# Performance work log

Hardware: AMD Instinct MI355X
Metric: run time of the kernel (lower is better)

The kernel has to match this reference:

```python
import jax, jax.numpy as jnp
import numpy as np

LN_EPS = 1e-5


def setup_inputs() -> dict:
    key = jax.random.key(0)
    ks = jax.random.split(key, 8)
    N, E, DIN, DOUT = 50000, 800000, 128, 128
    s = 1.0 / np.sqrt(DIN)
    return {
        "vertex_features": jax.random.normal(ks[0], (N, DIN), jnp.float32),
        "edge_index": jax.random.randint(ks[1], (2, E), 0, N, jnp.int32),
        "W_edge": jax.random.normal(ks[2], (DIN, DOUT), jnp.float32) * s,
        "b_edge": jnp.zeros((DOUT,), jnp.float32),
        "W1": jax.random.normal(ks[3], (DIN + DOUT, DOUT), jnp.float32) * (1.0 / np.sqrt(DIN + DOUT)),
        "b1": jnp.zeros((DOUT,), jnp.float32),
        "ln_gamma": jnp.ones((DOUT,), jnp.float32),
        "ln_beta": jnp.zeros((DOUT,), jnp.float32),
        "W2": jax.random.normal(ks[4], (DOUT, DOUT), jnp.float32) * (1.0 / np.sqrt(DOUT)),
        "b2": jnp.zeros((DOUT,), jnp.float32),
    }


def layer_norm(x, gamma, beta):
    mu = jnp.mean(x, axis=-1, keepdims=True)
    var = jnp.mean(jnp.square(x - mu), axis=-1, keepdims=True)
    return (x - mu) * jax.lax.rsqrt(var + LN_EPS) * gamma + beta


def reference(vertex_features, edge_index, W_edge, b_edge, W1, b1, ln_gamma, ln_beta, W2, b2):
    N = vertex_features.shape[0]
    src, dst = edge_index[0], edge_index[1]
    # gather-subtract: [E, DIN]
    edge_feats = vertex_features[src] - vertex_features[dst]
    # edge linear: [E, DOUT]
    edge_feats = edge_feats @ W_edge + b_edge
    # scatter_max by dst -> [N, DOUT]; empty segments get -inf -> replace with 0
    agg = jax.ops.segment_max(edge_feats, dst, num_segments=N)
    agg = jnp.where(jnp.isfinite(agg), agg, 0.0)
    combined = jnp.concatenate([vertex_features, agg], axis=-1)  # [N, DIN+DOUT]
    h = combined @ W1 + b1
    h = jax.nn.relu(layer_norm(h, ln_gamma, ln_beta))
    return h @ W2 + b2
```

## Files before the change

### kernel.cpp

```cpp
#include <hip/hip_runtime.h>
#include <stdint.h>

#define DIN 128
#define DOUT 128
#define LN_EPS 1e-5f
#define CAP 64

typedef __attribute__((ext_vector_type(8))) short bf16x8;
typedef __attribute__((ext_vector_type(4))) float f32x4;

__device__ __forceinline__ unsigned short f2bf(float f) {
  uint32_t u = __float_as_uint(f);
  uint32_t r = (u + 0x7fffu + ((u >> 16) & 1u)) >> 16;
  return (unsigned short)r;
}
__device__ __forceinline__ float bf2f(uint32_t lo16) {
  return __uint_as_float(lo16 << 16);
}
__device__ __forceinline__ uint32_t pack2(unsigned short a, unsigned short b) {
  return (uint32_t)a | ((uint32_t)b << 16);
}
__device__ __forceinline__ uint32_t cvtpk_bf16(float lo, float hi) {
  uint32_t r;
  asm volatile("v_cvt_pk_bf16_f32 %0, %1, %2" : "=v"(r) : "v"(lo), "v"(hi));
  return r;
}

__global__ __launch_bounds__(256) void k_prep(
    const float* __restrict__ We, const float* __restrict__ W1,
    const float* __restrict__ W2, char* __restrict__ img,
    int4* __restrict__ degv4, int nv4, int wblk) {
  if (blockIdx.x >= wblk) {
    int i = (blockIdx.x - wblk) * 256 + threadIdx.x;
    if (i < nv4) degv4[i] = make_int4(0, 0, 0, 0);
    return;
  }
  int tid = blockIdx.x * 256 + threadIdx.x;
  const int total = 128 * 128 + 256 * 128 + 128 * 128;
  for (int i = tid; i < total; i += wblk * 256) {
    int off;
    float v;
    if (i < 16384) {
      int k = i >> 7, c = i & 127;
      v = We[k * 128 + c];
      off = c * 256 + ((k * 2) ^ ((c & 7) << 4));
    } else if (i < 49152) {
      int j = i - 16384;
      int k = j >> 7, c = j & 127;
      v = W1[k * 128 + c];
      off = 32768 + c * 512 + ((k * 2) ^ ((c & 7) << 4));
    } else {
      int j = i - 49152;
      int k = j >> 7, c = j & 127;
      v = W2[k * 128 + c];
      off = 98304 + c * 256 + ((k * 2) ^ ((c & 7) << 4));
    }
    *(unsigned short*)(img + off) = f2bf(v);
  }
}

__global__ __launch_bounds__(256, 1) void k_gemm_histplace(
    const float* __restrict__ vf, const char* __restrict__ wimg,
    short* __restrict__ P16, short* __restrict__ vf16, int N,
    const int* __restrict__ ei, int* __restrict__ deg,
    unsigned short* __restrict__ ssrc, int E, int nblk) {
  __shared__ char Wet[32768];
  if (blockIdx.x >= nblk) {
    int e = (blockIdx.x - nblk) * 256 + threadIdx.x;
    if (e < E) {
      int s = ei[e];
      int d = ei[E + e];
      int r = atomicAdd(&deg[d], 1);
      if (r < CAP) ssrc[(size_t)d * CAP + r] = (unsigned short)s;
    }
    return;
  }
  {
    const uint4* src = (const uint4*)wimg;
    for (int i = threadIdx.x; i < 2048; i += 256) *(uint4*)(Wet + i * 16) = src[i];
  }
  int wave = threadIdx.x >> 6, lane = threadIdx.x & 63;
  int l15 = lane & 15, lq = lane >> 4;
  int row0 = blockIdx.x * 256 + wave * 64;
  int rs[4];
#pragma unroll
  for (int m = 0; m < 4; ++m) rs[m] = min(row0 + m * 16 + l15, N - 1);

  f32x4 acc[4][8];
#pragma unroll
  for (int m = 0; m < 4; ++m)
#pragma unroll
    for (int n = 0; n < 8; ++n) acc[m][n] = (f32x4)0.f;

  float4 pf0[4], pf1[4];
#pragma unroll
  for (int m = 0; m < 4; ++m) {
    const float* p = vf + (size_t)rs[m] * DIN + lq * 8;
    pf0[m] = *(const float4*)p;
    pf1[m] = *(const float4*)(p + 4);
  }
  __syncthreads();

#pragma unroll
  for (int ks = 0; ks < 4; ++ks) {
    bf16x8 afr[4];
#pragma unroll
    for (int m = 0; m < 4; ++m) {
      uint4 st;
      st.x = cvtpk_bf16(pf0[m].x, pf0[m].y);
      st.y = cvtpk_bf16(pf0[m].z, pf0[m].w);
      st.z = cvtpk_bf16(pf1[m].x, pf1[m].y);
      st.w = cvtpk_bf16(pf1[m].z, pf1[m].w);
      afr[m] = *(bf16x8*)&st;
      int row = row0 + m * 16 + l15;
      if (row < N)
        *(uint4*)(vf16 + (size_t)row * DIN + ks * 32 + lq * 8) = st;
    }
    if (ks < 3) {
#pragma unroll
      for (int m = 0; m < 4; ++m) {
        const float* p = vf + (size_t)rs[m] * DIN + (ks + 1) * 32 + lq * 8;
        pf0[m] = *(const float4*)p;
        pf1[m] = *(const float4*)(p + 4);
      }
    }
    int kb = ks * 64 + lq * 16;
#pragma unroll
    for (int n = 0; n < 8; ++n) {
      int c = n * 16 + l15;
      bf16x8 b = *(const bf16x8*)(Wet + c * 256 + (kb ^ ((c & 7) << 4)));
#pragma unroll
      for (int m = 0; m < 4; ++m)
        acc[m][n] = __builtin_amdgcn_mfma_f32_16x16x32_bf16(afr[m], b, acc[m][n], 0, 0, 0);
    }
  }
#pragma unroll
  for (int m = 0; m < 4; ++m) {
    int rbase = row0 + m * 16 + lq * 4;
#pragma unroll
    for (int n = 0; n < 8; ++n) {
      int col = n * 16 + l15;
#pragma unroll
      for (int reg = 0; reg < 4; ++reg) {
        int row = rbase + reg;
        if (row < N) P16[(size_t)row * DOUT + col] = (short)f2bf(acc[m][n][reg]);
      }
    }
  }
}

__global__ __launch_bounds__(256) void k_segmax(const short* __restrict__ P16,
                                                const int* __restrict__ degA,
                                                const unsigned short* __restrict__ ssrc,
                                                const float* __restrict__ b_edge,
                                                short* __restrict__ A16, int N) {
  int lane = threadIdx.x & 63;
  int l16 = lane & 15;
  int v = blockIdx.x * 16 + (threadIdx.x >> 4);
  if (v >= N) return;
  int deg = min(degA[v], CAP);
  size_t beg = (size_t)v * CAP;
  float m[8];
#pragma unroll
  for (int j = 0; j < 8; ++j) m[j] = -__builtin_inff();
  for (int r = 0; r < deg; r += 16) {
    int cnt = min(16, deg - r);
    int sv = (l16 < cnt) ? (int)ssrc[beg + r + l16] : 0;
#pragma unroll 2
    for (int i = 0; i < cnt; ++i) {
      int s = __shfl(sv, (lane & 48) + i, 64);
      uint4 p = *(const uint4*)(P16 + (size_t)s * DOUT + l16 * 8);
      m[0] = fmaxf(m[0], bf2f(p.x & 0xffffu));
      m[1] = fmaxf(m[1], bf2f(p.x >> 16));
      m[2] = fmaxf(m[2], bf2f(p.y & 0xffffu));
      m[3] = fmaxf(m[3], bf2f(p.y >> 16));
      m[4] = fmaxf(m[4], bf2f(p.z & 0xffffu));
      m[5] = fmaxf(m[5], bf2f(p.z >> 16));
      m[6] = fmaxf(m[6], bf2f(p.w & 0xffffu));
      m[7] = fmaxf(m[7], bf2f(p.w >> 16));
    }
  }
  uint4 pv = *(const uint4*)(P16 + (size_t)v * DOUT + l16 * 8);
  float4 be0 = *(const float4*)(b_edge + l16 * 8);
  float4 be1 = *(const float4*)(b_edge + l16 * 8 + 4);
  float pvf[8] = {bf2f(pv.x & 0xffffu), bf2f(pv.x >> 16), bf2f(pv.y & 0xffffu),
                  bf2f(pv.y >> 16),     bf2f(pv.z & 0xffffu), bf2f(pv.z >> 16),
                  bf2f(pv.w & 0xffffu), bf2f(pv.w >> 16)};
  float bev[8] = {be0.x, be0.y, be0.z, be0.w, be1.x, be1.y, be1.z, be1.w};
  uint32_t o[4];
#pragma unroll
  for (int j = 0; j < 4; ++j) {
    float a0 = (deg > 0) ? (m[2 * j] - pvf[2 * j] + bev[2 * j]) : 0.f;
    float a1 = (deg > 0) ? (m[2 * j + 1] - pvf[2 * j + 1] + bev[2 * j + 1]) : 0.f;
    o[j] = pack2(f2bf(a0), f2bf(a1));
  }
  *(uint4*)(A16 + (size_t)v * DOUT + l16 * 8) = *(uint4*)o;
}

__global__ __launch_bounds__(256, 1) void k_mlp12(
    const short* __restrict__ vf16, const short* __restrict__ A16,
    const char* __restrict__ wimg, const float* __restrict__ b1,
    const float* __restrict__ gamma, const float* __restrict__ beta,
    const float* __restrict__ b2, float* __restrict__ out, int N) {
  __shared__ char lds[98304];
  char* W1t = lds;
  char* W2t = lds + 65536;
  {
    const uint4* src = (const uint4*)(wimg + 32768);
    for (int i = threadIdx.x; i < 6144; i += 256) *(uint4*)(lds + i * 16) = src[i];
  }
  int wave = threadIdx.x >> 6, lane = threadIdx.x & 63;
  int l15 = lane & 15, lq = lane >> 4;
  int row0 = blockIdx.x * 256 + wave * 64;
  int rs[4];
#pragma unroll
  for (int m = 0; m < 4; ++m) rs[m] = min(row0 + m * 16 + l15, N - 1);
  float b1v[8], gv[8], bev[8], b2v[8];
#pragma unroll
  for (int n = 0; n < 8; ++n) {
    int c = n * 16 + l15;
    b1v[n] = b1[c];
    gv[n] = gamma[c];
    bev[n] = beta[c];
    b2v[n] = b2[c];
  }
  f32x4 acc[4][8];
#pragma unroll
  for (int m = 0; m < 4; ++m)
#pragma unroll
    for (int n = 0; n < 8; ++n) acc[m][n] = (f32x4)0.f;

  uint4 pa[4];
#pragma unroll
  for (int m = 0; m < 4; ++m)
    pa[m] = *(const uint4*)(vf16 + (size_t)rs[m] * DIN + lq * 8);
  __syncthreads();

#pragma unroll
  for (int ks = 0; ks < 8; ++ks) {
    bf16x8 afr[4];
#pragma unroll
    for (int m = 0; m < 4; ++m) afr[m] = *(bf16x8*)&pa[m];
    if (ks < 7) {
      int ks1 = ks + 1;
      const short* srcb = (ks1 < 4) ? vf16 : A16;
      int chunk = (ks1 < 4) ? ks1 : ks1 - 4;
#pragma unroll
      for (int m = 0; m < 4; ++m)
        pa[m] = *(const uint4*)(srcb + (size_t)rs[m] * DIN + chunk * 32 + lq * 8);
    }
    int kb = ks * 64 + lq * 16;
#pragma unroll
    for (int n = 0; n < 8; ++n) {
      int c = n * 16 + l15;
      bf16x8 b = *(const bf16x8*)(W1t + c * 512 + (kb ^ ((c & 7) << 4)));
#pragma unroll
      for (int m = 0; m < 4; ++m)
        acc[m][n] = __builtin_amdgcn_mfma_f32_16x16x32_bf16(afr[m], b, acc[m][n], 0, 0, 0);
    }
  }
  __syncthreads();

#pragma unroll
  for (int m = 0; m < 4; ++m) {
#pragma unroll
    for (int n = 0; n < 8; ++n)
#pragma unroll
      for (int reg = 0; reg < 4; ++reg) acc[m][n][reg] += b1v[n];
    float s[4], sq[4];
#pragma unroll
    for (int reg = 0; reg < 4; ++reg) {
      s[reg] = 0.f;
      sq[reg] = 0.f;
#pragma unroll
      for (int n = 0; n < 8; ++n) {
        float h = acc[m][n][reg];
        s[reg] += h;
        sq[reg] += h * h;
      }
    }
#pragma unroll
    for (int mm = 1; mm < 16; mm <<= 1) {
#pragma unroll
      for (int reg = 0; reg < 4; ++reg) {
        s[reg] += __shfl_xor(s[reg], mm, 64);
        sq[reg] += __shfl_xor(sq[reg], mm, 64);
      }
    }
#pragma unroll
    for (int reg = 0; reg < 4; ++reg) {
      float mu = s[reg] * (1.f / 128.f);
      float var = sq[reg] * (1.f / 128.f) - mu * mu;
      float rsn = rsqrtf(var + LN_EPS);
      int rr = wave * 64 + m * 16 + lq * 4 + reg;
#pragma unroll
      for (int n = 0; n < 8; ++n) {
        float o = fmaxf(fmaf((acc[m][n][reg] - mu) * rsn, gv[n], bev[n]), 0.f);
        int c = n * 16 + l15;
        *(unsigned short*)(W1t + rr * 256 + ((c * 2) ^ ((rr & 7) << 4))) = f2bf(o);
      }
    }
  }
  __syncthreads();

  f32x4 acc2[4][8];
#pragma unroll
  for (int m = 0; m < 4; ++m)
#pragma unroll
    for (int n = 0; n < 8; ++n) acc2[m][n] = (f32x4)0.f;
#pragma unroll
  for (int ks = 0; ks < 4; ++ks) {
    int kb = ks * 64 + lq * 16;
    bf16x8 a2[4];
#pragma unroll
    for (int m = 0; m < 4; ++m) {
      int rr = wave * 64 + m * 16 + l15;
      a2[m] = *(const bf16x8*)(W1t + rr * 256 + (kb ^ ((rr & 7) << 4)));
    }
#pragma unroll
    for (int n = 0; n < 8; ++n) {
      int c = n * 16 + l15;
      bf16x8 b = *(const bf16x8*)(W2t + c * 256 + (kb ^ ((c & 7) << 4)));
#pragma unroll
      for (int m = 0; m < 4; ++m)
        acc2[m][n] = __builtin_amdgcn_mfma_f32_16x16x32_bf16(a2[m], b, acc2[m][n], 0, 0, 0);
    }
  }
#pragma unroll
  for (int m = 0; m < 4; ++m) {
    int rbase = row0 + m * 16 + lq * 4;
#pragma unroll
    for (int n = 0; n < 8; ++n) {
      int col = n * 16 + l15;
#pragma unroll
      for (int reg = 0; reg < 4; ++reg) {
        int row = rbase + reg;
        if (row < N) out[(size_t)row * DOUT + col] = acc2[m][n][reg] + b2v[n];
      }
    }
  }
}

extern "C" void kernel_launch(void* const* d_in, const int* in_sizes, int n_in,
                              void* d_out, int out_size, void* d_ws, size_t ws_size,
                              hipStream_t stream) {
  const float* vf     = (const float*)d_in[0];
  const int*   ei     = (const int*)d_in[1];
  const float* W_edge = (const float*)d_in[2];
  const float* b_edge = (const float*)d_in[3];
  const float* W1     = (const float*)d_in[4];
  const float* b1     = (const float*)d_in[5];
  const float* gamma  = (const float*)d_in[6];
  const float* beta   = (const float*)d_in[7];
  const float* W2     = (const float*)d_in[8];
  const float* b2     = (const float*)d_in[9];
  float* out = (float*)d_out;

  int N = in_sizes[0] / DIN;
  int E = in_sizes[1] / 2;
  int nblk = (N + 255) / 256;
  int eblk = (E + 255) / 256;

  char* ws = (char*)d_ws;
  size_t seg16 = (size_t)N * DOUT * sizeof(short);
  short* P16  = (short*)ws;
  short* vf16 = (short*)(ws + seg16);
  short* A16  = (short*)(ws + 2 * seg16);
  char*  wimg = ws + 3 * seg16;
  int*   deg  = (int*)(ws + 3 * seg16 + 131072);
  unsigned short* ssrc = (unsigned short*)(deg + ((N + 3) & ~3));

  int nv4 = (N + 3) / 4;
  int zblk = (nv4 + 255) / 256;
  k_prep<<<64 + zblk, 256, 0, stream>>>(W_edge, W1, W2, wimg, (int4*)deg, nv4, 64);
  k_gemm_histplace<<<nblk + eblk, 256, 0, stream>>>(vf, wimg, P16, vf16, N, ei,
                                                    deg, ssrc, E, nblk);
  k_segmax<<<(N + 15) / 16, 256, 0, stream>>>(P16, deg, ssrc, b_edge, A16, N);
  k_mlp12<<<nblk, 256, 0, stream>>>(vf16, A16, wimg, b1, gamma, beta, b2, out, N);
}
```

Before: 114.5 us.

## Privatize edge histogram and bucket lists per XCD to avoid cross-die atomics

The shared degree counters and per-destination source lists are replaced with one copy per XCD, selected by reading the hardware XCC id register. Atomics are relaxed at workgroup scope, which is meant to remove cross-die coherence traffic and contention on the global counters. The segment-max kernel then walks all eight buckets per vertex and sums their counts. Edge blocks are also launched ahead of GEMM blocks. In exchange, workspace and zeroing grow eightfold, the source-list scatter spreads over a much larger footprint, and the reduction loop has more overhead per vertex.

```diff
diff --git a/kernel.cpp b/kernel.cpp
--- a/kernel.cpp
+++ b/kernel.cpp
@@ -4,7 +4,10 @@
 #define DIN 128
 #define DOUT 128
 #define LN_EPS 1e-5f
-#define CAP 64
+#define CAPX 64
+#define NXCD 8
+
+#define XCC_ID_ENC (20 | (0 << 6) | ((4 - 1) << 11))
 
 typedef __attribute__((ext_vector_type(8))) short bf16x8;
 typedef __attribute__((ext_vector_type(4))) float f32x4;
@@ -62,26 +65,30 @@
 __global__ __launch_bounds__(256, 1) void k_gemm_histplace(
     const float* __restrict__ vf, const char* __restrict__ wimg,
     short* __restrict__ P16, short* __restrict__ vf16, int N,
-    const int* __restrict__ ei, int* __restrict__ deg,
-    unsigned short* __restrict__ ssrc, int E, int nblk) {
+    const int* __restrict__ ei, int* __restrict__ deg8,
+    unsigned short* __restrict__ ssrc8, int E, int eblk) {
   __shared__ char Wet[32768];
-  if (blockIdx.x >= nblk) {
-    int e = (blockIdx.x - nblk) * 256 + threadIdx.x;
+  if (blockIdx.x < eblk) {
+    int e = blockIdx.x * 256 + threadIdx.x;
     if (e < E) {
       int s = ei[e];
       int d = ei[E + e];
-      int r = atomicAdd(&deg[d], 1);
-      if (r < CAP) ssrc[(size_t)d * CAP + r] = (unsigned short)s;
+      uint32_t xcc = ((uint32_t)__builtin_amdgcn_s_getreg(XCC_ID_ENC)) & (NXCD - 1);
+      int r = __hip_atomic_fetch_add(&deg8[(size_t)xcc * N + d], 1,
+                                     __ATOMIC_RELAXED, __HIP_MEMORY_SCOPE_WORKGROUP);
+      if (r < CAPX)
+        ssrc8[((size_t)xcc * N + d) * CAPX + r] = (unsigned short)s;
     }
     return;
   }
+  int bid = blockIdx.x - eblk;
   {
     const uint4* src = (const uint4*)wimg;
     for (int i = threadIdx.x; i < 2048; i += 256) *(uint4*)(Wet + i * 16) = src[i];
   }
   int wave = threadIdx.x >> 6, lane = threadIdx.x & 63;
   int l15 = lane & 15, lq = lane >> 4;
-  int row0 = blockIdx.x * 256 + wave * 64;
+  int row0 = bid * 256 + wave * 64;
   int rs[4];
 #pragma unroll
   for (int m = 0; m < 4; ++m) rs[m] = min(row0 + m * 16 + l15, N - 1);
@@ -150,34 +157,39 @@
 }
 
 __global__ __launch_bounds__(256) void k_segmax(const short* __restrict__ P16,
-                                                const int* __restrict__ degA,
-                                                const unsigned short* __restrict__ ssrc,
+                                                const int* __restrict__ deg8,
+                                                const unsigned short* __restrict__ ssrc8,
                                                 const float* __restrict__ b_edge,
                                                 short* __restrict__ A16, int N) {
   int lane = threadIdx.x & 63;
   int l16 = lane & 15;
   int v = blockIdx.x * 16 + (threadIdx.x >> 4);
   if (v >= N) return;
-  int deg = min(degA[v], CAP);
-  size_t beg = (size_t)v * CAP;
+  int cx = (l16 < NXCD) ? deg8[(size_t)l16 * N + v] : 0;
   float m[8];
 #pragma unroll
   for (int j = 0; j < 8; ++j) m[j] = -__builtin_inff();
-  for (int r = 0; r < deg; r += 16) {
-    int cnt = min(16, deg - r);
-    int sv = (l16 < cnt) ? (int)ssrc[beg + r + l16] : 0;
+  int total = 0;
+  for (int x = 0; x < NXCD; ++x) {
+    int cnt = min(__shfl(cx, (lane & 48) + x, 64), CAPX);
+    total += cnt;
+    size_t base = ((size_t)x * N + v) * CAPX;
+    for (int r = 0; r < cnt; r += 16) {
+      int c2 = min(16, cnt - r);
+      int sv = (l16 < c2) ? (int)ssrc8[base + r + l16] : 0;
 #pragma unroll 2
-    for (int i = 0; i < cnt; ++i) {
-      int s = __shfl(sv, (lane & 48) + i, 64);
-      uint4 p = *(const uint4*)(P16 + (size_t)s * DOUT + l16 * 8);
-      m[0] = fmaxf(m[0], bf2f(p.x & 0xffffu));
-      m[1] = fmaxf(m[1], bf2f(p.x >> 16));
-      m[2] = fmaxf(m[2], bf2f(p.y & 0xffffu));
-      m[3] = fmaxf(m[3], bf2f(p.y >> 16));
-      m[4] = fmaxf(m[4], bf2f(p.z & 0xffffu));
-      m[5] = fmaxf(m[5], bf2f(p.z >> 16));
-      m[6] = fmaxf(m[6], bf2f(p.w & 0xffffu));
-      m[7] = fmaxf(m[7], bf2f(p.w >> 16));
+      for (int i = 0; i < c2; ++i) {
+        int s = __shfl(sv, (lane & 48) + i, 64);
+        uint4 p = *(const uint4*)(P16 + (size_t)s * DOUT + l16 * 8);
+        m[0] = fmaxf(m[0], bf2f(p.x & 0xffffu));
+        m[1] = fmaxf(m[1], bf2f(p.x >> 16));
+        m[2] = fmaxf(m[2], bf2f(p.y & 0xffffu));
+        m[3] = fmaxf(m[3], bf2f(p.y >> 16));
+        m[4] = fmaxf(m[4], bf2f(p.z & 0xffffu));
+        m[5] = fmaxf(m[5], bf2f(p.z >> 16));
+        m[6] = fmaxf(m[6], bf2f(p.w & 0xffffu));
+        m[7] = fmaxf(m[7], bf2f(p.w >> 16));
+      }
     }
   }
   uint4 pv = *(const uint4*)(P16 + (size_t)v * DOUT + l16 * 8);
@@ -190,8 +202,8 @@
   uint32_t o[4];
 #pragma unroll
   for (int j = 0; j < 4; ++j) {
-    float a0 = (deg > 0) ? (m[2 * j] - pvf[2 * j] + bev[2 * j]) : 0.f;
-    float a1 = (deg > 0) ? (m[2 * j + 1] - pvf[2 * j + 1] + bev[2 * j + 1]) : 0.f;
+    float a0 = (total > 0) ? (m[2 * j] - pvf[2 * j] + bev[2 * j]) : 0.f;
+    float a1 = (total > 0) ? (m[2 * j + 1] - pvf[2 * j + 1] + bev[2 * j + 1]) : 0.f;
     o[j] = pack2(f2bf(a0), f2bf(a1));
   }
   *(uint4*)(A16 + (size_t)v * DOUT + l16 * 8) = *(uint4*)o;
@@ -367,14 +379,15 @@
   short* vf16 = (short*)(ws + seg16);
   short* A16  = (short*)(ws + 2 * seg16);
   char*  wimg = ws + 3 * seg16;
-  int*   deg  = (int*)(ws + 3 * seg16 + 131072);
-  unsigned short* ssrc = (unsigned short*)(deg + ((N + 3) & ~3));
-
-  int nv4 = (N + 3) / 4;
+  int*   deg8 = (int*)(ws + 3 * seg16 + 131072);
+  unsigned short* ssrc8 =
+      (unsigned short*)(deg8 + (((size_t)NXCD * N + 3) & ~(size_t)3));
+
+  int nv4 = (NXCD * N + 3) / 4;
   int zblk = (nv4 + 255) / 256;
-  k_prep<<<64 + zblk, 256, 0, stream>>>(W_edge, W1, W2, wimg, (int4*)deg, nv4, 64);
-  k_gemm_histplace<<<nblk + eblk, 256, 0, stream>>>(vf, wimg, P16, vf16, N, ei,
-                                                    deg, ssrc, E, nblk);
-  k_segmax<<<(N + 15) / 16, 256, 0, stream>>>(P16, deg, ssrc, b_edge, A16, N);
+  k_prep<<<64 + zblk, 256, 0, stream>>>(W_edge, W1, W2, wimg, (int4*)deg8, nv4, 64);
+  k_gemm_histplace<<<eblk + nblk, 256, 0, stream>>>(vf, wimg, P16, vf16, N, ei,
+                                                    deg8, ssrc8, E, eblk);
+  k_segmax<<<(N + 15) / 16, 256, 0, stream>>>(P16, deg8, ssrc8, b_edge, A16, N);
   k_mlp12<<<nblk, 256, 0, stream>>>(vf16, A16, wimg, b1, gamma, beta, b2, out, N);
 }
```

Result: slower. 126.7 us (+10.6%).

## Replace per-vertex global atomic bucketing with two-level LDS binning of edges

Applied to the files above, without the earlier changes.

Edges are now binned by destination block. Each binning block takes a 16K-edge chunk, counts it into 256-vertex bins with LDS atomics and staging, then reserves space per bin with one global atomic. The segment-max kernel then rebuilds per-vertex source lists in LDS from each bin's list before gathering. This removes the 800K global atomics on a degree array and the zeroing of that array. It adds staging capacity limits (SCAP, BCAP, VCAP) that could silently drop edges under skewed distributions, and segmax now re-reads each bin's list four times.

```diff
diff --git a/kernel.cpp b/kernel.cpp
--- a/kernel.cpp
+++ b/kernel.cpp
@@ -4,7 +4,10 @@
 #define DIN 128
 #define DOUT 128
 #define LN_EPS 1e-5f
-#define CAP 64
+#define BCAP 6144
+#define SCAP 160
+#define VCAP 64
+#define CHUNK 16384
 
 typedef __attribute__((ext_vector_type(8))) short bf16x8;
 typedef __attribute__((ext_vector_type(4))) float f32x4;
@@ -29,15 +32,13 @@
 __global__ __launch_bounds__(256) void k_prep(
     const float* __restrict__ We, const float* __restrict__ W1,
     const float* __restrict__ W2, char* __restrict__ img,
-    int4* __restrict__ degv4, int nv4, int wblk) {
-  if (blockIdx.x >= wblk) {
-    int i = (blockIdx.x - wblk) * 256 + threadIdx.x;
-    if (i < nv4) degv4[i] = make_int4(0, 0, 0, 0);
-    return;
+    int* __restrict__ gcur, int NB) {
+  if (blockIdx.x == 0) {
+    for (int i = threadIdx.x; i < NB; i += 256) gcur[i] = 0;
   }
   int tid = blockIdx.x * 256 + threadIdx.x;
   const int total = 128 * 128 + 256 * 128 + 128 * 128;
-  for (int i = tid; i < total; i += wblk * 256) {
+  for (int i = tid; i < total; i += gridDim.x * 256) {
     int off;
     float v;
     if (i < 16384) {
@@ -59,29 +60,55 @@
   }
 }
 
-__global__ __launch_bounds__(256, 1) void k_gemm_histplace(
+__global__ __launch_bounds__(256, 1) void k_gemm_binA(
     const float* __restrict__ vf, const char* __restrict__ wimg,
     short* __restrict__ P16, short* __restrict__ vf16, int N,
-    const int* __restrict__ ei, int* __restrict__ deg,
-    unsigned short* __restrict__ ssrc, int E, int nblk) {
-  __shared__ char Wet[32768];
-  if (blockIdx.x >= nblk) {
-    int e = (blockIdx.x - nblk) * 256 + threadIdx.x;
-    if (e < E) {
-      int s = ei[e];
-      int d = ei[E + e];
-      int r = atomicAdd(&deg[d], 1);
-      if (r < CAP) ssrc[(size_t)d * CAP + r] = (unsigned short)s;
+    const int* __restrict__ ei, int* __restrict__ gcur,
+    uint32_t* __restrict__ gbuf, int E, int nbin) {
+  __shared__ char lds[126464];
+  if (blockIdx.x < nbin) {
+    int* cnt = (int*)lds;
+    uint32_t* stage = (uint32_t*)(lds + 1024);
+    int NB = (N + 255) >> 8;
+    for (int i = threadIdx.x; i < NB; i += 256) cnt[i] = 0;
+    __syncthreads();
+    int c0 = blockIdx.x * CHUNK;
+#pragma unroll 4
+    for (int t = 0; t < CHUNK / 256; ++t) {
+      int e = c0 + t * 256 + threadIdx.x;
+      if (e < E) {
+        int s = ei[e];
+        int d = ei[E + e];
+        int b = d >> 8;
+        int r = atomicAdd(&cnt[b], 1);
+        if (r < SCAP)
+          stage[b * SCAP + r] = ((uint32_t)(d & 255) << 16) | (uint32_t)s;
+      }
+    }
+    __syncthreads();
+    if (threadIdx.x < NB) {
+      int c = min(cnt[threadIdx.x], SCAP);
+      if (c > 0) {
+        int base = atomicAdd(&gcur[threadIdx.x], c);
+        uint32_t* dst = gbuf + (size_t)threadIdx.x * BCAP;
+        const uint32_t* src = stage + threadIdx.x * SCAP;
+        for (int i = 0; i < c; ++i) {
+          int p = base + i;
+          if (p < BCAP) dst[p] = src[i];
+        }
+      }
     }
     return;
   }
+  char* Wet = lds;
+  int bid = blockIdx.x - nbin;
   {
     const uint4* src = (const uint4*)wimg;
     for (int i = threadIdx.x; i < 2048; i += 256) *(uint4*)(Wet + i * 16) = src[i];
   }
   int wave = threadIdx.x >> 6, lane = threadIdx.x & 63;
   int l15 = lane & 15, lq = lane >> 4;
-  int row0 = blockIdx.x * 256 + wave * 64;
+  int row0 = bid * 256 + wave * 64;
   int rs[4];
 #pragma unroll
   for (int m = 0; m < 4; ++m) rs[m] = min(row0 + m * 16 + l15, N - 1);
@@ -149,52 +176,72 @@
   }
 }
 
-__global__ __launch_bounds__(256) void k_segmax(const short* __restrict__ P16,
-                                                const int* __restrict__ degA,
-                                                const unsigned short* __restrict__ ssrc,
-                                                const float* __restrict__ b_edge,
-                                                short* __restrict__ A16, int N) {
+__global__ __launch_bounds__(256) void k_segmax2(
+    const short* __restrict__ P16, const int* __restrict__ gcur,
+    const uint32_t* __restrict__ gbuf, const float* __restrict__ b_edge,
+    short* __restrict__ A16, int N) {
+  __shared__ unsigned short vbin[64 * VCAP];
+  __shared__ int vcnt[64];
+  int b = blockIdx.x >> 2, q = blockIdx.x & 3;
+  if (threadIdx.x < 64) vcnt[threadIdx.x] = 0;
+  __syncthreads();
+  int cb = min(gcur[b], BCAP);
+  const uint32_t* list = gbuf + (size_t)b * BCAP;
+  for (int i = threadIdx.x; i < cb; i += 256) {
+    uint32_t u = list[i];
+    int vl8 = u >> 16;
+    if ((vl8 >> 6) == q) {
+      int vloc = vl8 & 63;
+      int r = atomicAdd(&vcnt[vloc], 1);
+      if (r < VCAP) vbin[vloc * VCAP + r] = (unsigned short)(u & 0xffffu);
+    }
+  }
+  __syncthreads();
   int lane = threadIdx.x & 63;
   int l16 = lane & 15;
-  int v = blockIdx.x * 16 + (threadIdx.x >> 4);
-  if (v >= N) return;
-  int deg = min(degA[v], CAP);
-  size_t beg = (size_t)v * CAP;
-  float m[8];
-#pragma unroll
-  for (int j = 0; j < 8; ++j) m[j] = -__builtin_inff();
-  for (int r = 0; r < deg; r += 16) {
-    int cnt = min(16, deg - r);
-    int sv = (l16 < cnt) ? (int)ssrc[beg + r + l16] : 0;
+  int gid = threadIdx.x >> 4;
+#pragma unroll
+  for (int k = 0; k < 4; ++k) {
+    int vloc = gid + k * 16;
+    int v = (b << 8) + (q << 6) + vloc;
+    if (v >= N) continue;
+    int deg = min(vcnt[vloc], VCAP);
+    float m[8];
+#pragma unroll
+    for (int j = 0; j < 8; ++j) m[j] = -__builtin_inff();
+    for (int r = 0; r < deg; r += 16) {
+      int c2 = min(16, deg - r);
+      int sv = (l16 < c2) ? (int)vbin[vloc * VCAP + r + l16] : 0;
 #pragma unroll 2
-    for (int i = 0; i < cnt; ++i) {
-      int s = __shfl(sv, (lane & 48) + i, 64);
-      uint4 p = *(const uint4*)(P16 + (size_t)s * DOUT + l16 * 8);
-      m[0] = fmaxf(m[0], bf2f(p.x & 0xffffu));
-      m[1] = fmaxf(m[1], bf2f(p.x >> 16));
-      m[2] = fmaxf(m[2], bf2f(p.y & 0xffffu));
-      m[3] = fmaxf(m[3], bf2f(p.y >> 16));
-      m[4] = fmaxf(m[4], bf2f(p.z & 0xffffu));
-      m[5] = fmaxf(m[5], bf2f(p.z >> 16));
-      m[6] = fmaxf(m[6], bf2f(p.w & 0xffffu));
-      m[7] = fmaxf(m[7], bf2f(p.w >> 16));
-    }
-  }
-  uint4 pv = *(const uint4*)(P16 + (size_t)v * DOUT + l16 * 8);
-  float4 be0 = *(const float4*)(b_edge + l16 * 8);
-  float4 be1 = *(const float4*)(b_edge + l16 * 8 + 4);
-  float pvf[8] = {bf2f(pv.x & 0xffffu), bf2f(pv.x >> 16), bf2f(pv.y & 0xffffu),
-                  bf2f(pv.y >> 16),     bf2f(pv.z & 0xffffu), bf2f(pv.z >> 16),
-                  bf2f(pv.w & 0xffffu), bf2f(pv.w >> 16)};
-  float bev[8] = {be0.x, be0.y, be0.z, be0.w, be1.x, be1.y, be1.z, be1.w};
-  uint32_t o[4];
-#pragma unroll
-  for (int j = 0; j < 4; ++j) {
-    float a0 = (deg > 0) ? (m[2 * j] - pvf[2 * j] + bev[2 * j]) : 0.f;
-    float a1 = (deg > 0) ? (m[2 * j + 1] - pvf[2 * j + 1] + bev[2 * j + 1]) : 0.f;
-    o[j] = pack2(f2bf(a0), f2bf(a1));
-  }
-  *(uint4*)(A16 + (size_t)v * DOUT + l16 * 8) = *(uint4*)o;
+      for (int i = 0; i < c2; ++i) {
+        int s = __shfl(sv, (lane & 48) + i, 64);
+        uint4 p = *(const uint4*)(P16 + (size_t)s * DOUT + l16 * 8);
+        m[0] = fmaxf(m[0], bf2f(p.x & 0xffffu));
+        m[1] = fmaxf(m[1], bf2f(p.x >> 16));
+        m[2] = fmaxf(m[2], bf2f(p.y & 0xffffu));
+        m[3] = fmaxf(m[3], bf2f(p.y >> 16));
+        m[4] = fmaxf(m[4], bf2f(p.z & 0xffffu));
+        m[5] = fmaxf(m[5], bf2f(p.z >> 16));
+        m[6] = fmaxf(m[6], bf2f(p.w & 0xffffu));
+        m[7] = fmaxf(m[7], bf2f(p.w >> 16));
+      }
+    }
+    uint4 pv = *(const uint4*)(P16 + (size_t)v * DOUT + l16 * 8);
+    float4 be0 = *(const float4*)(b_edge + l16 * 8);
+    float4 be1 = *(const float4*)(b_edge + l16 * 8 + 4);
+    float pvf[8] = {bf2f(pv.x & 0xffffu), bf2f(pv.x >> 16), bf2f(pv.y & 0xffffu),
+                    bf2f(pv.y >> 16),     bf2f(pv.z & 0xffffu), bf2f(pv.z >> 16),
+                    bf2f(pv.w & 0xffffu), bf2f(pv.w >> 16)};
+    float bev[8] = {be0.x, be0.y, be0.z, be0.w, be1.x, be1.y, be1.z, be1.w};
+    uint32_t o[4];
+#pragma unroll
+    for (int j = 0; j < 4; ++j) {
+      float a0 = (deg > 0) ? (m[2 * j] - pvf[2 * j] + bev[2 * j]) : 0.f;
+      float a1 = (deg > 0) ? (m[2 * j + 1] - pvf[2 * j + 1] + bev[2 * j + 1]) : 0.f;
+      o[j] = pack2(f2bf(a0), f2bf(a1));
+    }
+    *(uint4*)(A16 + (size_t)v * DOUT + l16 * 8) = *(uint4*)o;
+  }
 }
 
 __global__ __launch_bounds__(256, 1) void k_mlp12(
@@ -359,7 +406,8 @@
   int N = in_sizes[0] / DIN;
   int E = in_sizes[1] / 2;
   int nblk = (N + 255) / 256;
-  int eblk = (E + 255) / 256;
+  int NB = nblk;
+  int nbin = (E + CHUNK - 1) / CHUNK;
 
   char* ws = (char*)d_ws;
   size_t seg16 = (size_t)N * DOUT * sizeof(short);
@@ -367,14 +415,13 @@
   short* vf16 = (short*)(ws + seg16);
   short* A16  = (short*)(ws + 2 * seg16);
   char*  wimg = ws + 3 * seg16;
-  int*   deg  = (int*)(ws + 3 * seg16 + 131072);
-  unsigned short* ssrc = (unsigned short*)(deg + ((N + 3) & ~3));
-
-  int nv4 = (N + 3) / 4;
-  int zblk = (nv4 + 255) / 256;
-  k_prep<<<64 + zblk, 256, 0, stream>>>(W_edge, W1, W2, wimg, (int4*)deg, nv4, 64);
-  k_gemm_histplace<<<nblk + eblk, 256, 0, stream>>>(vf, wimg, P16, vf16, N, ei,
-                                                    deg, ssrc, E, nblk);
-  k_segmax<<<(N + 15) / 16, 256, 0, stream>>>(P16, deg, ssrc, b_edge, A16, N);
+  int*   gcur = (int*)(ws + 3 * seg16 + 131072);
+  uint32_t* gbuf = (uint32_t*)(ws + 3 * seg16 + 131072 +
+                               (((size_t)NB * 4 + 15) & ~(size_t)15));
+
+  k_prep<<<64, 256, 0, stream>>>(W_edge, W1, W2, wimg, gcur, NB);
+  k_gemm_binA<<<nbin + nblk, 256, 0, stream>>>(vf, wimg, P16, vf16, N, ei,
+                                               gcur, gbuf, E, nbin);
+  k_segmax2<<<NB * 4, 256, 0, stream>>>(P16, gcur, gbuf, b_edge, A16, N);
   k_mlp12<<<nblk, 256, 0, stream>>>(vf16, A16, wimg, b1, gamma, beta, b2, out, N);
 }
```

New measurement: 137.1 us. +19.7%, slower.

## Halve MLP tile rows and split W1 LDS staging to allow two blocks per CU

Applied to the files above, without the earlier changes.

The fused MLP kernel now processes 128 rows per block instead of 256 and stages W1 into LDS in two K-halves, reloading the second half mid-loop. This cuts LDS use from 96KB to 64KB and the accumulator registers by half, and launch bounds request two blocks per CU. The aim is more occupancy and more blocks across CUs to hide global-load latency. In exchange W1 is staged twice per block with extra barriers, and each weight fragment read from LDS feeds fewer MFMAs.

```diff
diff --git a/kernel.cpp b/kernel.cpp
--- a/kernel.cpp
+++ b/kernel.cpp
@@ -197,24 +197,28 @@
   *(uint4*)(A16 + (size_t)v * DOUT + l16 * 8) = *(uint4*)o;
 }
 
-__global__ __launch_bounds__(256, 1) void k_mlp12(
+__global__ __launch_bounds__(256, 2) void k_mlp12(
     const short* __restrict__ vf16, const short* __restrict__ A16,
     const char* __restrict__ wimg, const float* __restrict__ b1,
     const float* __restrict__ gamma, const float* __restrict__ beta,
     const float* __restrict__ b2, float* __restrict__ out, int N) {
-  __shared__ char lds[98304];
-  char* W1t = lds;
-  char* W2t = lds + 65536;
+  __shared__ char lds[65536];
+  char* W1h = lds;
+  char* W2t = lds + 32768;
   {
-    const uint4* src = (const uint4*)(wimg + 32768);
-    for (int i = threadIdx.x; i < 6144; i += 256) *(uint4*)(lds + i * 16) = src[i];
+    const uint4* wsrc = (const uint4*)wimg;
+    for (int i = threadIdx.x; i < 2048; i += 256) {
+      int c = i >> 4, x = i & 15;
+      ((uint4*)W1h)[i] = wsrc[2048 + c * 32 + x];
+      ((uint4*)W2t)[i] = wsrc[6144 + i];
+    }
   }
   int wave = threadIdx.x >> 6, lane = threadIdx.x & 63;
   int l15 = lane & 15, lq = lane >> 4;
-  int row0 = blockIdx.x * 256 + wave * 64;
-  int rs[4];
-#pragma unroll
-  for (int m = 0; m < 4; ++m) rs[m] = min(row0 + m * 16 + l15, N - 1);
+  int row0 = blockIdx.x * 128 + wave * 32;
+  int rs[2];
+#pragma unroll
+  for (int m = 0; m < 2; ++m) rs[m] = min(row0 + m * 16 + l15, N - 1);
   float b1v[8], gv[8], bev[8], b2v[8];
 #pragma unroll
   for (int n = 0; n < 8; ++n) {
@@ -224,45 +228,54 @@
     bev[n] = beta[c];
     b2v[n] = b2[c];
   }
-  f32x4 acc[4][8];
-#pragma unroll
-  for (int m = 0; m < 4; ++m)
+  f32x4 acc[2][8];
+#pragma unroll
+  for (int m = 0; m < 2; ++m)
 #pragma unroll
     for (int n = 0; n < 8; ++n) acc[m][n] = (f32x4)0.f;
 
-  uint4 pa[4];
-#pragma unroll
-  for (int m = 0; m < 4; ++m)
+  uint4 pa[2];
+#pragma unroll
+  for (int m = 0; m < 2; ++m)
     pa[m] = *(const uint4*)(vf16 + (size_t)rs[m] * DIN + lq * 8);
   __syncthreads();
 
 #pragma unroll
   for (int ks = 0; ks < 8; ++ks) {
-    bf16x8 afr[4];
-#pragma unroll
-    for (int m = 0; m < 4; ++m) afr[m] = *(bf16x8*)&pa[m];
+    if (ks == 4) {
+      __syncthreads();
+      const uint4* wsrc = (const uint4*)wimg;
+      for (int i = threadIdx.x; i < 2048; i += 256) {
+        int c = i >> 4, x = i & 15;
+        ((uint4*)W1h)[i] = wsrc[2048 + c * 32 + 16 + x];
+      }
+      __syncthreads();
+    }
+    bf16x8 afr[2];
+#pragma unroll
+    for (int m = 0; m < 2; ++m) afr[m] = *(bf16x8*)&pa[m];
     if (ks < 7) {
       int ks1 = ks + 1;
       const short* srcb = (ks1 < 4) ? vf16 : A16;
       int chunk = (ks1 < 4) ? ks1 : ks1 - 4;
 #pragma unroll
-      for (int m = 0; m < 4; ++m)
+      for (int m = 0; m < 2; ++m)
         pa[m] = *(const uint4*)(srcb + (size_t)rs[m] * DIN + chunk * 32 + lq * 8);
     }
-    int kb = ks * 64 + lq * 16;
+    int kb = (ks & 3) * 64 + lq * 16;
 #pragma unroll
     for (int n = 0; n < 8; ++n) {
       int c = n * 16 + l15;
-      bf16x8 b = *(const bf16x8*)(W1t + c * 512 + (kb ^ ((c & 7) << 4)));
-#pragma unroll
-      for (int m = 0; m < 4; ++m)
+      bf16x8 b = *(const bf16x8*)(W1h + c * 256 + (kb ^ ((c & 7) << 4)));
+#pragma unroll
+      for (int m = 0; m < 2; ++m)
         acc[m][n] = __builtin_amdgcn_mfma_f32_16x16x32_bf16(afr[m], b, acc[m][n], 0, 0, 0);
     }
   }
   __syncthreads();
 
 #pragma unroll
-  for (int m = 0; m < 4; ++m) {
+  for (int m = 0; m < 2; ++m) {
 #pragma unroll
     for (int n = 0; n < 8; ++n)
 #pragma unroll
@@ -292,42 +305,42 @@
       float mu = s[reg] * (1.f / 128.f);
       float var = sq[reg] * (1.f / 128.f) - mu * mu;
       float rsn = rsqrtf(var + LN_EPS);
-      int rr = wave * 64 + m * 16 + lq * 4 + reg;
+      int rr = wave * 32 + m * 16 + lq * 4 + reg;
 #pragma unroll
       for (int n = 0; n < 8; ++n) {
         float o = fmaxf(fmaf((acc[m][n][reg] - mu) * rsn, gv[n], bev[n]), 0.f);
         int c = n * 16 + l15;
-        *(unsigned short*)(W1t + rr * 256 + ((c * 2) ^ ((rr & 7) << 4))) = f2bf(o);
+        *(unsigned short*)(W1h + rr * 256 + ((c * 2) ^ ((rr & 7) << 4))) = f2bf(o);
       }
     }
   }
   __syncthreads();
 
-  f32x4 acc2[4][8];
-#pragma unroll
-  for (int m = 0; m < 4; ++m)
+  f32x4 acc2[2][8];
+#pragma unroll
+  for (int m = 0; m < 2; ++m)
 #pragma unroll
     for (int n = 0; n < 8; ++n) acc2[m][n] = (f32x4)0.f;
 #pragma unroll
   for (int ks = 0; ks < 4; ++ks) {
     int kb = ks * 64 + lq * 16;
-    bf16x8 a2[4];
-#pragma unroll
-    for (int m = 0; m < 4; ++m) {
-      int rr = wave * 64 + m * 16 + l15;
-      a2[m] = *(const bf16x8*)(W1t + rr * 256 + (kb ^ ((rr & 7) << 4)));
+    bf16x8 a2[2];
+#pragma unroll
+    for (int m = 0; m < 2; ++m) {
+      int rr = wave * 32 + m * 16 + l15;
+      a2[m] = *(const bf16x8*)(W1h + rr * 256 + (kb ^ ((rr & 7) << 4)));
     }
 #pragma unroll
     for (int n = 0; n < 8; ++n) {
       int c = n * 16 + l15;
       bf16x8 b = *(const bf16x8*)(W2t + c * 256 + (kb ^ ((c & 7) << 4)));
 #pragma unroll
-      for (int m = 0; m < 4; ++m)
+      for (int m = 0; m < 2; ++m)
         acc2[m][n] = __builtin_amdgcn_mfma_f32_16x16x32_bf16(a2[m], b, acc2[m][n], 0, 0, 0);
     }
   }
 #pragma unroll
-  for (int m = 0; m < 4; ++m) {
+  for (int m = 0; m < 2; ++m) {
     int rbase = row0 + m * 16 + lq * 4;
 #pragma unroll
     for (int n = 0; n < 8; ++n) {
@@ -360,6 +373,7 @@
   int E = in_sizes[1] / 2;
   int nblk = (N + 255) / 256;
   int eblk = (E + 255) / 256;
+  int mblk = (N + 127) / 128;
 
   char* ws = (char*)d_ws;
   size_t seg16 = (size_t)N * DOUT * sizeof(short);
@@ -376,5 +390,5 @@
   k_gemm_histplace<<<nblk + eblk, 256, 0, stream>>>(vf, wimg, P16, vf16, N, ei,
                                                     deg, ssrc, E, nblk);
   k_segmax<<<(N + 15) / 16, 256, 0, stream>>>(P16, deg, ssrc, b_edge, A16, N);
-  k_mlp12<<<nblk, 256, 0, stream>>>(vf16, A16, wimg, b1, gamma, beta, b2, out, N);
-}
+  k_mlp12<<<mblk, 256, 0, stream>>>(vf16, A16, wimg, b1, gamma, beta, b2, out, N);
+}
```

After: 109.3 us. 4.5% less time.
